# Performance work log

Hardware: AMD Instinct MI355X
Metric: run time of the kernel (lower is better)

Reference implementation:

```python
import jax, jax.numpy as jnp
import numpy as np

N, E, L, S = 20000, 100000, 128, 6   # nodes, edges, latent, message-passing steps
NF, EF, TW, OUT = 11, 5, 5, 1        # node feat, edge feat, time_window, output_size
LN_EPS = 1e-5


def _mlp_ln(x, W1, b1, W2, b2, g, beta):
    # Linear -> ReLU -> Linear -> ReLU -> LayerNorm (matches torch Sequential)
    h = jax.nn.relu(x @ W1 + b1)
    h = jax.nn.relu(h @ W2 + b2)
    mu = h.mean(-1, keepdims=True)
    var = ((h - mu) ** 2).mean(-1, keepdims=True)
    return (h - mu) * jax.lax.rsqrt(var + LN_EPS) * g + beta


def setup_inputs() -> dict:
    key = jax.random.key(0)
    ks = iter(jax.random.split(key, 64))

    def w(shape):
        fan_in = shape[-2]
        return jax.random.normal(next(ks), shape, jnp.float32) / np.float32(np.sqrt(fan_in))

    inp = {
        'node_features': jax.random.normal(next(ks), (1, N, NF), jnp.float32),
        'edge_features': jax.random.normal(next(ks), (1, E, EF), jnp.float32),
        'senders': jax.random.randint(next(ks), (E,), 0, N, jnp.int32),
        'receivers': jax.random.randint(next(ks), (E,), 0, N, jnp.int32),
        'node_mean': jax.random.normal(next(ks), (NF,), jnp.float32),
        'node_std': jnp.ones((NF,), jnp.float32),
        'edge_mean': jax.random.normal(next(ks), (EF,), jnp.float32),
        'edge_std': jnp.ones((EF,), jnp.float32),
        'enc_n_W1': w((NF, L)), 'enc_n_b1': jnp.zeros((L,), jnp.float32),
        'enc_n_W2': w((L, L)), 'enc_n_b2': jnp.zeros((L,), jnp.float32),
        'enc_n_g': jnp.ones((L,), jnp.float32), 'enc_n_beta': jnp.zeros((L,), jnp.float32),
        'enc_e_W1': w((EF, L)), 'enc_e_b1': jnp.zeros((L,), jnp.float32),
        'enc_e_W2': w((L, L)), 'enc_e_b2': jnp.zeros((L,), jnp.float32),
        'enc_e_g': jnp.ones((L,), jnp.float32), 'enc_e_beta': jnp.zeros((L,), jnp.float32),
        'blk_e_W1': w((S, 3 * L, L)), 'blk_e_b1': jnp.zeros((S, L), jnp.float32),
        'blk_e_W2': w((S, L, L)), 'blk_e_b2': jnp.zeros((S, L), jnp.float32),
        'blk_e_g': jnp.ones((S, L), jnp.float32), 'blk_e_beta': jnp.zeros((S, L), jnp.float32),
        'blk_n_W1': w((S, 2 * L, L)), 'blk_n_b1': jnp.zeros((S, L), jnp.float32),
        'blk_n_W2': w((S, L, L)), 'blk_n_b2': jnp.zeros((S, L), jnp.float32),
        'blk_n_g': jnp.ones((S, L), jnp.float32), 'blk_n_beta': jnp.zeros((S, L), jnp.float32),
        'dec_W1': w((L, 8)), 'dec_b1': jnp.zeros((8,), jnp.float32),
        'dec_W2': w((8, TW)), 'dec_b2': jnp.zeros((TW,), jnp.float32),
    }
    return inp


def reference(node_features, edge_features, senders, receivers,
              node_mean, node_std, edge_mean, edge_std,
              enc_n_W1, enc_n_b1, enc_n_W2, enc_n_b2, enc_n_g, enc_n_beta,
              enc_e_W1, enc_e_b1, enc_e_W2, enc_e_b2, enc_e_g, enc_e_beta,
              blk_e_W1, blk_e_b1, blk_e_W2, blk_e_b2, blk_e_g, blk_e_beta,
              blk_n_W1, blk_n_b1, blk_n_W2, blk_n_b2, blk_n_g, blk_n_beta,
              dec_W1, dec_b1, dec_W2, dec_b2):
    # ---- encode (Normalizer in eval mode: (x - mean) / std) ----
    node_lat = _mlp_ln((node_features - node_mean) / node_std,
                       enc_n_W1, enc_n_b1, enc_n_W2, enc_n_b2, enc_n_g, enc_n_beta)  # [1,N,L]
    edge_lat = _mlp_ln((edge_features - edge_mean) / edge_std,
                       enc_e_W1, enc_e_b1, enc_e_W2, enc_e_b2, enc_e_g, enc_e_beta)  # [1,E,L]

    # ---- process: gather -> edge MLP -> scatter_add -> node MLP, residuals ----
    for i in range(S):
        e_in = jnp.concatenate([node_lat[:, senders, :], node_lat[:, receivers, :], edge_lat], axis=-1)  # [1,E,3L]
        new_e = _mlp_ln(e_in, blk_e_W1[i], blk_e_b1[i], blk_e_W2[i], blk_e_b2[i], blk_e_g[i], blk_e_beta[i])
        aggr = jax.ops.segment_sum(new_e[0], receivers, num_segments=N)[None]  # [1,N,L]
        new_n = _mlp_ln(jnp.concatenate([node_lat, aggr], axis=-1),
                        blk_n_W1[i], blk_n_b1[i], blk_n_W2[i], blk_n_b2[i], blk_n_g[i], blk_n_beta[i])
        node_lat = node_lat + new_n
        edge_lat = edge_lat + new_e

    # ---- decode: Conv1d(k=1) == per-node linear; Swish(beta=1) ----
    h = node_lat[0] @ dec_W1 + dec_b1          # [N,8]
    h = h * jax.nn.sigmoid(h)
    dec = h @ dec_W2 + dec_b2                  # [N,TW]
    dt = jnp.repeat(jnp.arange(1, TW + 1), OUT).astype(dec.dtype)  # [TW*OUT]
    delta = (dec * dt).reshape(N, TW, OUT).transpose(1, 0, 2)      # [TW,N,OUT]
    return delta
```

## Files before the change

kernel.cpp:

```cpp
#include <hip/hip_runtime.h>
#include <cstdint>
#include <cstddef>


#define N_NODES 20000
#define N_EDGES 100000
#define LDIM    128
#define NSTEPS  6

typedef float  f32x4  __attribute__((ext_vector_type(4)));
typedef __bf16 bf16x8 __attribute__((ext_vector_type(8)));
typedef __bf16 bf16x2 __attribute__((ext_vector_type(2)));

__device__ __forceinline__ bf16x8 cvt8(const float* p) {
  float4 u = *(const float4*)p;
  float4 v = *(const float4*)(p + 4);
  bf16x8 o;
  o[0] = (__bf16)u.x; o[1] = (__bf16)u.y; o[2] = (__bf16)u.z; o[3] = (__bf16)u.w;
  o[4] = (__bf16)v.x; o[5] = (__bf16)v.y; o[6] = (__bf16)v.z; o[7] = (__bf16)v.w;
  return o;
}

struct PrepArgs {
  const float *s_enW1, *s_enW2, *s_eeW1, *s_eeW2;
  const float *s_beW1, *s_beW2, *s_bnW1, *s_bnW2;
  __bf16 *d_enW1, *d_enW2, *d_eeW1, *d_eeW2;
  __bf16 *d_beW1, *d_beW2, *d_bnW1, *d_bnW2;
  int* counts;
};

__device__ __forceinline__ void swz_src(int idx, int& k, int& col) {
  int j    = idx & 7;
  int lane = (idx >> 3) & 63;
  int ct   = (idx >> 9) & 7;
  int kc   = idx >> 12;
  col = ct * 16 + (lane & 15);
  k   = kc * 32 + (lane >> 4) * 8 + j;
}

__global__ __launch_bounds__(256) void prep_kernel(PrepArgs p) {
  int idx = blockIdx.x * 256 + threadIdx.x;
  int k, col;

  if (idx < 4096) {
    swz_src(idx, k, col);
    p.d_enW1[idx] = (__bf16)((k < 11) ? p.s_enW1[k * 128 + col] : 0.f);
    return;
  }
  idx -= 4096;
  if (idx < 16384) {
    swz_src(idx, k, col);
    p.d_enW2[idx] = (__bf16)p.s_enW2[k * 128 + col];
    return;
  }
  idx -= 16384;
  if (idx < 4096) {
    swz_src(idx, k, col);
    p.d_eeW1[idx] = (__bf16)((k < 5) ? p.s_eeW1[k * 128 + col] : 0.f);
    return;
  }
  idx -= 4096;
  if (idx < 16384) {
    swz_src(idx, k, col);
    p.d_eeW2[idx] = (__bf16)p.s_eeW2[k * 128 + col];
    return;
  }
  idx -= 16384;
  if (idx < 294912) {
    int s = idx / 49152, rem = idx % 49152;
    swz_src(rem, k, col);
    p.d_beW1[idx] = (__bf16)p.s_beW1[(size_t)s * 49152 + k * 128 + col];
    return;
  }
  idx -= 294912;
  if (idx < 98304) {
    int s = idx >> 14, rem = idx & 16383;
    swz_src(rem, k, col);
    p.d_beW2[idx] = (__bf16)p.s_beW2[s * 16384 + k * 128 + col];
    return;
  }
  idx -= 98304;
  if (idx < 196608) {
    int s = idx >> 15, rem = idx & 32767;
    swz_src(rem, k, col);
    p.d_bnW1[idx] = (__bf16)p.s_bnW1[s * 32768 + k * 128 + col];
    return;
  }
  idx -= 196608;
  if (idx < 98304) {
    int s = idx >> 14, rem = idx & 16383;
    swz_src(rem, k, col);
    p.d_bnW2[idx] = (__bf16)p.s_bnW2[s * 16384 + k * 128 + col];
    return;
  }
  idx -= 98304;
  if (idx < N_NODES) p.counts[idx] = 0;
}

__global__ __launch_bounds__(256) void hist_kernel(const int* __restrict__ recv,
                                                   int* __restrict__ counts) {
  int e = blockIdx.x * 256 + threadIdx.x;
  if (e < N_EDGES) atomicAdd(&counts[recv[e]], 1);
}

__global__ __launch_bounds__(1024) void scan_kernel(const int* __restrict__ counts,
                                                    int* __restrict__ row_ptr,
                                                    int* __restrict__ cursor) {
  __shared__ int part[1024];
  const int t = threadIdx.x;
  const int base = t * 20;
  int local[20];
  int s = 0;
#pragma unroll
  for (int i = 0; i < 20; ++i) {
    int idx = base + i;
    int v = (idx < N_NODES) ? counts[idx] : 0;
    local[i] = s;
    s += v;
  }
  part[t] = s;
  __syncthreads();
  for (int off = 1; off < 1024; off <<= 1) {
    int add = (t >= off) ? part[t - off] : 0;
    __syncthreads();
    part[t] += add;
    __syncthreads();
  }
  const int excl = part[t] - s;
#pragma unroll
  for (int i = 0; i < 20; ++i) {
    int idx = base + i;
    if (idx < N_NODES) {
      int v = excl + local[i];
      row_ptr[idx] = v;
      cursor[idx]  = v;
    }
  }
  if (t == 1023) row_ptr[N_NODES] = part[1023];
}

__global__ __launch_bounds__(256) void fill_kernel(const int* __restrict__ recv,
                                                   int* __restrict__ cursor,
                                                   int* __restrict__ edge_list) {
  int e = blockIdx.x * 256 + threadIdx.x;
  if (e < N_EDGES) {
    int r = recv[e];
    int pos = atomicAdd(&cursor[r], 1);
    edge_list[pos] = e;
  }
}

__global__ __launch_bounds__(256) void agg_kernel(
    const int* __restrict__ row_ptr, const int* __restrict__ edge_list,
    const __bf16* __restrict__ new_e, __bf16* __restrict__ aggr_bf) {
  const int wv   = threadIdx.x >> 6;
  const int lane = threadIdx.x & 63;
  const int n    = blockIdx.x * 4 + wv;
  if (n >= N_NODES) return;
  int p = row_ptr[n];
  const int pe = row_ptr[n + 1];
  float s0 = 0.f, s1 = 0.f;
  while (p < pe) {
    const int cnt = min(pe - p, 64);
    int eid = (lane < cnt) ? edge_list[p + lane] : 0;
    for (int j = 0; j < cnt; ++j) {
      const int e = __shfl(eid, j);
      bf16x2 v = *(const bf16x2*)(new_e + (size_t)e * LDIM + lane * 2);
      s0 += (float)v[0];
      s1 += (float)v[1];
    }
    p += cnt;
  }
  bf16x2 o;
  o[0] = (__bf16)s0; o[1] = (__bf16)s1;
  *(bf16x2*)(aggr_bf + (size_t)n * LDIM + lane * 2) = o;
}

struct MlpArgs {
  const float* x; const float* mean; const float* stdv;
  float* node_lat; float* edge_lat;
  __bf16* new_e;
  const __bf16* aggr_bf;
  const int* senders; const int* receivers;
  const __bf16* W1t; const __bf16* W2t;
  const float* b1; const float* b2; const float* g; const float* beta;
  int M;
};

template <int K1, int MODE>
__global__ __launch_bounds__(256, 3) void mlp2_kernel(MlpArgs a) {
  constexpr int NKC = K1 / 32;
  constexpr int RT  = 2;
  constexpr int HS  = 136;

  __shared__ __align__(16) __bf16 H1[4 * 32 * HS];

  const int tid   = threadIdx.x;
  const int lane  = tid & 63;
  const int wv    = tid >> 6;
  const int l15   = lane & 15;
  const int quad  = lane >> 4;
  const int M     = a.M;
  const int rbase = blockIdx.x * 128 + wv * 32;

  __bf16* h1w = H1 + wv * 32 * HS;

  int rowA[RT];
#pragma unroll
  for (int rt = 0; rt < RT; ++rt) {
    int r = rbase + rt * 16 + l15;
    rowA[rt] = (r < M) ? r : (M - 1);
  }

  int sA[RT], rA[RT];
  if constexpr (MODE == 2) {
#pragma unroll
    for (int rt = 0; rt < RT; ++rt) {
      sA[rt] = a.senders[rowA[rt]];
      rA[rt] = a.receivers[rowA[rt]];
    }
  }

  f32x4 acc[RT][8];
#pragma unroll
  for (int rt = 0; rt < RT; ++rt)
#pragma unroll
    for (int i = 0; i < 8; ++i) acc[rt][i] = (f32x4)(0.f);

#pragma unroll
  for (int kc = 0; kc < NKC; ++kc) {
    bf16x8 af[RT];
    if constexpr (MODE == 0 || MODE == 1) {
      constexpr int KIN = (MODE == 0) ? 11 : 5;
#pragma unroll
      for (int rt = 0; rt < RT; ++rt) {
        const float* xr = a.x + (size_t)rowA[rt] * KIN;
#pragma unroll
        for (int j = 0; j < 8; ++j) {
          int c = quad * 8 + j;
          float v = (c < KIN) ? (xr[c] - a.mean[c]) / a.stdv[c] : 0.f;
          af[rt][j] = (__bf16)v;
        }
      }
    } else if constexpr (MODE == 2) {
      if (kc < 4) {
#pragma unroll
        for (int rt = 0; rt < RT; ++rt)
          af[rt] = cvt8(a.node_lat + (size_t)sA[rt] * LDIM + kc * 32 + quad * 8);
      } else if (kc < 8) {
#pragma unroll
        for (int rt = 0; rt < RT; ++rt)
          af[rt] = cvt8(a.node_lat + (size_t)rA[rt] * LDIM + (kc - 4) * 32 + quad * 8);
      } else {
#pragma unroll
        for (int rt = 0; rt < RT; ++rt)
          af[rt] = cvt8(a.edge_lat + (size_t)rowA[rt] * LDIM + (kc - 8) * 32 + quad * 8);
      }
    } else {
      if (kc < 4) {
#pragma unroll
        for (int rt = 0; rt < RT; ++rt)
          af[rt] = cvt8(a.node_lat + (size_t)rowA[rt] * LDIM + kc * 32 + quad * 8);
      } else {
#pragma unroll
        for (int rt = 0; rt < RT; ++rt)
          af[rt] = *(const bf16x8*)(a.aggr_bf + (size_t)rowA[rt] * LDIM + (kc - 4) * 32 + quad * 8);
      }
    }

    bf16x8 bf[8];
#pragma unroll
    for (int ct = 0; ct < 8; ++ct)
      bf[ct] = *(const bf16x8*)(a.W1t + ((kc * 8 + ct) * 64 + lane) * 8);

#pragma unroll
    for (int rt = 0; rt < RT; ++rt)
#pragma unroll
      for (int ct = 0; ct < 8; ++ct)
        acc[rt][ct] = __builtin_amdgcn_mfma_f32_16x16x32_bf16(af[rt], bf[ct], acc[rt][ct], 0, 0, 0);
  }

#pragma unroll
  for (int ct = 0; ct < 8; ++ct) {
    const float bb = a.b1[ct * 16 + l15];
#pragma unroll
    for (int rt = 0; rt < RT; ++rt)
#pragma unroll
      for (int rr = 0; rr < 4; ++rr) {
        float v = fmaxf(acc[rt][ct][rr] + bb, 0.f);
        h1w[(rt * 16 + quad * 4 + rr) * HS + ct * 16 + l15] = (__bf16)v;
      }
  }

#pragma unroll
  for (int rt = 0; rt < RT; ++rt)
#pragma unroll
    for (int i = 0; i < 8; ++i) acc[rt][i] = (f32x4)(0.f);

#pragma unroll
  for (int kc = 0; kc < 4; ++kc) {
    bf16x8 af[RT];
#pragma unroll
    for (int rt = 0; rt < RT; ++rt)
      af[rt] = *(const bf16x8*)(h1w + (rt * 16 + l15) * HS + kc * 32 + quad * 8);
    bf16x8 bf[8];
#pragma unroll
    for (int ct = 0; ct < 8; ++ct)
      bf[ct] = *(const bf16x8*)(a.W2t + ((kc * 8 + ct) * 64 + lane) * 8);
#pragma unroll
    for (int rt = 0; rt < RT; ++rt)
#pragma unroll
      for (int ct = 0; ct < 8; ++ct)
        acc[rt][ct] = __builtin_amdgcn_mfma_f32_16x16x32_bf16(af[rt], bf[ct], acc[rt][ct], 0, 0, 0);
  }

#pragma unroll
  for (int ct = 0; ct < 8; ++ct) {
    const float bb = a.b2[ct * 16 + l15];
#pragma unroll
    for (int rt = 0; rt < RT; ++rt)
#pragma unroll
      for (int rr = 0; rr < 4; ++rr)
        acc[rt][ct][rr] = fmaxf(acc[rt][ct][rr] + bb, 0.f);
  }

  float mu[RT][4], rs[RT][4];
#pragma unroll
  for (int rt = 0; rt < RT; ++rt)
#pragma unroll
    for (int rr = 0; rr < 4; ++rr) {
      float s = 0.f, s2 = 0.f;
#pragma unroll
      for (int ct = 0; ct < 8; ++ct) { float v = acc[rt][ct][rr]; s += v; s2 += v * v; }
      s  += __shfl_xor(s, 1);  s2 += __shfl_xor(s2, 1);
      s  += __shfl_xor(s, 2);  s2 += __shfl_xor(s2, 2);
      s  += __shfl_xor(s, 4);  s2 += __shfl_xor(s2, 4);
      s  += __shfl_xor(s, 8);  s2 += __shfl_xor(s2, 8);
      float m = s * (1.f / 128.f);
      float var = fmaxf(s2 * (1.f / 128.f) - m * m, 0.f);
      mu[rt][rr] = m; rs[rt][rr] = rsqrtf(var + 1e-5f);
    }

  float gv[8], bev[8];
#pragma unroll
  for (int ct = 0; ct < 8; ++ct) {
    gv[ct]  = a.g[ct * 16 + l15];
    bev[ct] = a.beta[ct * 16 + l15];
  }

#pragma unroll
  for (int rt = 0; rt < RT; ++rt)
#pragma unroll
    for (int rr = 0; rr < 4; ++rr) {
      const int row = rbase + rt * 16 + quad * 4 + rr;
      if (row >= M) continue;
      if constexpr (MODE == 2) {
#pragma unroll
        for (int ct = 0; ct < 8; ++ct) {
          const int col = ct * 16 + l15;
          float y = (acc[rt][ct][rr] - mu[rt][rr]) * rs[rt][rr] * gv[ct] + bev[ct];
          a.edge_lat[(size_t)row * LDIM + col] += y;
          a.new_e[(size_t)row * LDIM + col] = (__bf16)y;
        }
      } else {
#pragma unroll
        for (int ct = 0; ct < 8; ++ct) {
          const int col = ct * 16 + l15;
          float y = (acc[rt][ct][rr] - mu[rt][rr]) * rs[rt][rr] * gv[ct] + bev[ct];
          if constexpr (MODE == 0)      a.node_lat[(size_t)row * LDIM + col] = y;
          else if constexpr (MODE == 1) a.edge_lat[(size_t)row * LDIM + col] = y;
          else                          a.node_lat[(size_t)row * LDIM + col] += y;
        }
      }
    }
}

__global__ __launch_bounds__(256) void decode_kernel(
    const float* __restrict__ node_lat,
    const float* __restrict__ W1, const float* __restrict__ b1,
    const float* __restrict__ W2, const float* __restrict__ b2,
    float* __restrict__ out) {
  __shared__ float X[64][129];
  const int n0 = blockIdx.x * 64;
  for (int idx = threadIdx.x; idx < 64 * 32; idx += 256) {
    int r = idx >> 5, c4 = idx & 31;
    int n = n0 + r; if (n >= N_NODES) n = N_NODES - 1;
    float4 v = *((const float4*)(node_lat + (size_t)n * 128) + c4);
    X[r][c4 * 4 + 0] = v.x; X[r][c4 * 4 + 1] = v.y;
    X[r][c4 * 4 + 2] = v.z; X[r][c4 * 4 + 3] = v.w;
  }
  __syncthreads();
  const int r = threadIdx.x;
  if (r < 64) {
    const int n = n0 + r;
    if (n < N_NODES) {
      float h[8];
#pragma unroll
      for (int j = 0; j < 8; ++j) h[j] = b1[j];
      for (int k = 0; k < 128; ++k) {
        float xv = X[r][k];
#pragma unroll
        for (int j = 0; j < 8; ++j) h[j] = fmaf(xv, W1[k * 8 + j], h[j]);
      }
#pragma unroll
      for (int j = 0; j < 8; ++j) h[j] = h[j] / (1.f + expf(-h[j]));
#pragma unroll
      for (int t = 0; t < 5; ++t) {
        float d = b2[t];
#pragma unroll
        for (int j = 0; j < 8; ++j) d = fmaf(h[j], W2[j * 5 + t], d);
        out[t * N_NODES + n] = d * (float)(t + 1);
      }
    }
  }
}

extern "C" void kernel_launch(void* const* d_in, const int* in_sizes, int n_in,
                              void* d_out, int out_size, void* d_ws, size_t ws_size,
                              hipStream_t stream) {
  (void)in_sizes; (void)n_in; (void)out_size; (void)ws_size;

  const float* node_features = (const float*)d_in[0];
  const float* edge_features = (const float*)d_in[1];
  const int*   senders       = (const int*)d_in[2];
  const int*   receivers     = (const int*)d_in[3];
  const float* node_mean = (const float*)d_in[4];
  const float* node_std  = (const float*)d_in[5];
  const float* edge_mean = (const float*)d_in[6];
  const float* edge_std  = (const float*)d_in[7];
  const float* enc_n_W1 = (const float*)d_in[8];
  const float* enc_n_b1 = (const float*)d_in[9];
  const float* enc_n_W2 = (const float*)d_in[10];
  const float* enc_n_b2 = (const float*)d_in[11];
  const float* enc_n_g    = (const float*)d_in[12];
  const float* enc_n_beta = (const float*)d_in[13];
  const float* enc_e_W1 = (const float*)d_in[14];
  const float* enc_e_b1 = (const float*)d_in[15];
  const float* enc_e_W2 = (const float*)d_in[16];
  const float* enc_e_b2 = (const float*)d_in[17];
  const float* enc_e_g    = (const float*)d_in[18];
  const float* enc_e_beta = (const float*)d_in[19];
  const float* blk_e_W1 = (const float*)d_in[20];
  const float* blk_e_b1 = (const float*)d_in[21];
  const float* blk_e_W2 = (const float*)d_in[22];
  const float* blk_e_b2 = (const float*)d_in[23];
  const float* blk_e_g    = (const float*)d_in[24];
  const float* blk_e_beta = (const float*)d_in[25];
  const float* blk_n_W1 = (const float*)d_in[26];
  const float* blk_n_b1 = (const float*)d_in[27];
  const float* blk_n_W2 = (const float*)d_in[28];
  const float* blk_n_b2 = (const float*)d_in[29];
  const float* blk_n_g    = (const float*)d_in[30];
  const float* blk_n_beta = (const float*)d_in[31];
  const float* dec_W1 = (const float*)d_in[32];
  const float* dec_b1 = (const float*)d_in[33];
  const float* dec_W2 = (const float*)d_in[34];
  const float* dec_b2 = (const float*)d_in[35];

  char* ws = (char*)d_ws;
  float*  node_lat = (float*)(ws);
  float*  edge_lat = (float*)(ws + 10240000);
  __bf16* new_e    = (__bf16*)(ws + 61440000);
  __bf16* wb       = (__bf16*)(ws + 87040000);
  int* counts    = (int*)(ws + 88498176);
  int* row_ptr   = (int*)(ws + 88578176);
  int* cursor    = (int*)(ws + 88658192);
  int* edge_list = (int*)(ws + 88738192);
  __bf16* aggr_bf = (__bf16*)(ws + 89138192);

  __bf16* enW1s = wb;
  __bf16* enW2s = enW1s + 4096;
  __bf16* eeW1s = enW2s + 16384;
  __bf16* eeW2s = eeW1s + 4096;
  __bf16* beW1s = eeW2s + 16384;
  __bf16* beW2s = beW1s + 6 * 49152;
  __bf16* bnW1s = beW2s + 6 * 16384;
  __bf16* bnW2s = bnW1s + 6 * 32768;

  PrepArgs pa;
  pa.s_enW1 = enc_n_W1; pa.s_enW2 = enc_n_W2; pa.s_eeW1 = enc_e_W1; pa.s_eeW2 = enc_e_W2;
  pa.s_beW1 = blk_e_W1; pa.s_beW2 = blk_e_W2; pa.s_bnW1 = blk_n_W1; pa.s_bnW2 = blk_n_W2;
  pa.d_enW1 = enW1s; pa.d_enW2 = enW2s; pa.d_eeW1 = eeW1s; pa.d_eeW2 = eeW2s;
  pa.d_beW1 = beW1s; pa.d_beW2 = beW2s; pa.d_bnW1 = bnW1s; pa.d_bnW2 = bnW2s;
  pa.counts = counts;
  prep_kernel<<<2927, 256, 0, stream>>>(pa);

  hist_kernel<<<(N_EDGES + 255) / 256, 256, 0, stream>>>(receivers, counts);
  scan_kernel<<<1, 1024, 0, stream>>>(counts, row_ptr, cursor);
  fill_kernel<<<(N_EDGES + 255) / 256, 256, 0, stream>>>(receivers, cursor, edge_list);

  const int NODE_BLOCKS = (N_NODES + 127) / 128;
  const int EDGE_BLOCKS = (N_EDGES + 127) / 128;
  const int DEC_BLOCKS  = (N_NODES + 63) / 64;
  const int AGG_BLOCKS  = (N_NODES + 3) / 4;

  MlpArgs base;
  base.node_lat = node_lat; base.edge_lat = edge_lat; base.new_e = new_e;
  base.aggr_bf = aggr_bf;
  base.senders = senders; base.receivers = receivers;
  base.x = nullptr; base.mean = nullptr; base.stdv = nullptr;

  {
    MlpArgs a = base;
    a.x = node_features; a.mean = node_mean; a.stdv = node_std;
    a.W1t = enW1s; a.W2t = enW2s;
    a.b1 = enc_n_b1; a.b2 = enc_n_b2; a.g = enc_n_g; a.beta = enc_n_beta;
    a.M = N_NODES;
    mlp2_kernel<32, 0><<<NODE_BLOCKS, 256, 0, stream>>>(a);
  }
  {
    MlpArgs a = base;
    a.x = edge_features; a.mean = edge_mean; a.stdv = edge_std;
    a.W1t = eeW1s; a.W2t = eeW2s;
    a.b1 = enc_e_b1; a.b2 = enc_e_b2; a.g = enc_e_g; a.beta = enc_e_beta;
    a.M = N_EDGES;
    mlp2_kernel<32, 1><<<EDGE_BLOCKS, 256, 0, stream>>>(a);
  }

  for (int i = 0; i < NSTEPS; ++i) {
    {
      MlpArgs a = base;
      a.W1t = beW1s + (size_t)i * 49152; a.W2t = beW2s + (size_t)i * 16384;
      a.b1 = blk_e_b1 + i * 128; a.b2 = blk_e_b2 + i * 128;
      a.g = blk_e_g + i * 128; a.beta = blk_e_beta + i * 128;
      a.M = N_EDGES;
      mlp2_kernel<384, 2><<<EDGE_BLOCKS, 256, 0, stream>>>(a);
    }
    agg_kernel<<<AGG_BLOCKS, 256, 0, stream>>>(row_ptr, edge_list, new_e, aggr_bf);
    {
      MlpArgs a = base;
      a.W1t = bnW1s + (size_t)i * 32768; a.W2t = bnW2s + (size_t)i * 16384;
      a.b1 = blk_n_b1 + i * 128; a.b2 = blk_n_b2 + i * 128;
      a.g = blk_n_g + i * 128; a.beta = blk_n_beta + i * 128;
      a.M = N_NODES;
      mlp2_kernel<256, 3><<<NODE_BLOCKS, 256, 0, stream>>>(a);
    }
  }

  decode_kernel<<<DEC_BLOCKS, 256, 0, stream>>>(
      node_lat, dec_W1, dec_b1, dec_W2, dec_b2, (float*)d_out);
}
```

Baseline: 782.2 us.

## Use single-wave MLP blocks and batch activation gathers per 128-wide phase

Each MLP block now holds a single 64-thread wavefront handling 32 rows instead of four waves handling 128, and the grid grows to match. The first GEMM's activation loads are regrouped so that all four k-chunks of a 128-wide segment (sender, receiver, edge, or aggr) are issued before the MFMAs run. This exposes more memory-level parallelism per wave for the gather loads. In exchange, register pressure rises because more fragments are live at once, and with launch_bounds(64,3) occupancy now depends on per-block LDS and the VGPR count.

```diff
diff --git a/kernel.cpp b/kernel.cpp
--- a/kernel.cpp
+++ b/kernel.cpp
@@ -188,22 +188,20 @@
 };
 
 template <int K1, int MODE>
-__global__ __launch_bounds__(256, 3) void mlp2_kernel(MlpArgs a) {
+__global__ __launch_bounds__(64, 3) void mlp2_kernel(MlpArgs a) {
   constexpr int NKC = K1 / 32;
   constexpr int RT  = 2;
   constexpr int HS  = 136;
 
-  __shared__ __align__(16) __bf16 H1[4 * 32 * HS];
-
-  const int tid   = threadIdx.x;
-  const int lane  = tid & 63;
-  const int wv    = tid >> 6;
+  __shared__ __align__(16) __bf16 H1[32 * HS];
+
+  const int lane  = threadIdx.x & 63;
   const int l15   = lane & 15;
   const int quad  = lane >> 4;
   const int M     = a.M;
-  const int rbase = blockIdx.x * 128 + wv * 32;
-
-  __bf16* h1w = H1 + wv * 32 * HS;
+  const int rbase = blockIdx.x * 32;
+
+  __bf16* h1w = H1;
 
   int rowA[RT];
 #pragma unroll
@@ -227,57 +225,64 @@
 #pragma unroll
     for (int i = 0; i < 8; ++i) acc[rt][i] = (f32x4)(0.f);
 
-#pragma unroll
-  for (int kc = 0; kc < NKC; ++kc) {
+  if constexpr (MODE == 0 || MODE == 1) {
+    constexpr int KIN = (MODE == 0) ? 11 : 5;
     bf16x8 af[RT];
-    if constexpr (MODE == 0 || MODE == 1) {
-      constexpr int KIN = (MODE == 0) ? 11 : 5;
-#pragma unroll
-      for (int rt = 0; rt < RT; ++rt) {
-        const float* xr = a.x + (size_t)rowA[rt] * KIN;
-#pragma unroll
-        for (int j = 0; j < 8; ++j) {
-          int c = quad * 8 + j;
-          float v = (c < KIN) ? (xr[c] - a.mean[c]) / a.stdv[c] : 0.f;
-          af[rt][j] = (__bf16)v;
+#pragma unroll
+    for (int rt = 0; rt < RT; ++rt) {
+      const float* xr = a.x + (size_t)rowA[rt] * KIN;
+#pragma unroll
+      for (int j = 0; j < 8; ++j) {
+        int c = quad * 8 + j;
+        float v = (c < KIN) ? (xr[c] - a.mean[c]) / a.stdv[c] : 0.f;
+        af[rt][j] = (__bf16)v;
+      }
+    }
+    bf16x8 bfv[8];
+#pragma unroll
+    for (int ct = 0; ct < 8; ++ct)
+      bfv[ct] = *(const bf16x8*)(a.W1t + (ct * 64 + lane) * 8);
+#pragma unroll
+    for (int rt = 0; rt < RT; ++rt)
+#pragma unroll
+      for (int ct = 0; ct < 8; ++ct)
+        acc[rt][ct] = __builtin_amdgcn_mfma_f32_16x16x32_bf16(af[rt], bfv[ct], acc[rt][ct], 0, 0, 0);
+  } else {
+    constexpr int NPH = NKC / 4;
+#pragma unroll
+    for (int ph = 0; ph < NPH; ++ph) {
+      bf16x8 afr[RT][4];
+#pragma unroll
+      for (int kk = 0; kk < 4; ++kk) {
+#pragma unroll
+        for (int rt = 0; rt < RT; ++rt) {
+          if constexpr (MODE == 2) {
+            const float* src = (ph == 0) ? (a.node_lat + (size_t)sA[rt] * LDIM)
+                             : (ph == 1) ? (a.node_lat + (size_t)rA[rt] * LDIM)
+                                         : (a.edge_lat + (size_t)rowA[rt] * LDIM);
+            afr[rt][kk] = cvt8(src + kk * 32 + quad * 8);
+          } else {
+            if (ph == 0)
+              afr[rt][kk] = cvt8(a.node_lat + (size_t)rowA[rt] * LDIM + kk * 32 + quad * 8);
+            else
+              afr[rt][kk] = *(const bf16x8*)(a.aggr_bf + (size_t)rowA[rt] * LDIM + kk * 32 + quad * 8);
+          }
         }
       }
-    } else if constexpr (MODE == 2) {
-      if (kc < 4) {
+#pragma unroll
+      for (int kk = 0; kk < 4; ++kk) {
+        const int kc = ph * 4 + kk;
+        bf16x8 bfv[8];
+#pragma unroll
+        for (int ct = 0; ct < 8; ++ct)
+          bfv[ct] = *(const bf16x8*)(a.W1t + ((kc * 8 + ct) * 64 + lane) * 8);
 #pragma unroll
         for (int rt = 0; rt < RT; ++rt)
-          af[rt] = cvt8(a.node_lat + (size_t)sA[rt] * LDIM + kc * 32 + quad * 8);
-      } else if (kc < 8) {
-#pragma unroll
-        for (int rt = 0; rt < RT; ++rt)
-          af[rt] = cvt8(a.node_lat + (size_t)rA[rt] * LDIM + (kc - 4) * 32 + quad * 8);
-      } else {
-#pragma unroll
-        for (int rt = 0; rt < RT; ++rt)
-          af[rt] = cvt8(a.edge_lat + (size_t)rowA[rt] * LDIM + (kc - 8) * 32 + quad * 8);
-      }
-    } else {
-      if (kc < 4) {
-#pragma unroll
-        for (int rt = 0; rt < RT; ++rt)
-          af[rt] = cvt8(a.node_lat + (size_t)rowA[rt] * LDIM + kc * 32 + quad * 8);
-      } else {
-#pragma unroll
-        for (int rt = 0; rt < RT; ++rt)
-          af[rt] = *(const bf16x8*)(a.aggr_bf + (size_t)rowA[rt] * LDIM + (kc - 4) * 32 + quad * 8);
-      }
-    }
-
-    bf16x8 bf[8];
-#pragma unroll
-    for (int ct = 0; ct < 8; ++ct)
-      bf[ct] = *(const bf16x8*)(a.W1t + ((kc * 8 + ct) * 64 + lane) * 8);
-
-#pragma unroll
-    for (int rt = 0; rt < RT; ++rt)
-#pragma unroll
-      for (int ct = 0; ct < 8; ++ct)
-        acc[rt][ct] = __builtin_amdgcn_mfma_f32_16x16x32_bf16(af[rt], bf[ct], acc[rt][ct], 0, 0, 0);
+#pragma unroll
+          for (int ct = 0; ct < 8; ++ct)
+            acc[rt][ct] = __builtin_amdgcn_mfma_f32_16x16x32_bf16(afr[rt][kk], bfv[ct], acc[rt][ct], 0, 0, 0);
+      }
+    }
   }
 
 #pragma unroll
@@ -303,15 +308,15 @@
 #pragma unroll
     for (int rt = 0; rt < RT; ++rt)
       af[rt] = *(const bf16x8*)(h1w + (rt * 16 + l15) * HS + kc * 32 + quad * 8);
-    bf16x8 bf[8];
+    bf16x8 bfv[8];
 #pragma unroll
     for (int ct = 0; ct < 8; ++ct)
-      bf[ct] = *(const bf16x8*)(a.W2t + ((kc * 8 + ct) * 64 + lane) * 8);
+      bfv[ct] = *(const bf16x8*)(a.W2t + ((kc * 8 + ct) * 64 + lane) * 8);
 #pragma unroll
     for (int rt = 0; rt < RT; ++rt)
 #pragma unroll
       for (int ct = 0; ct < 8; ++ct)
-        acc[rt][ct] = __builtin_amdgcn_mfma_f32_16x16x32_bf16(af[rt], bf[ct], acc[rt][ct], 0, 0, 0);
+        acc[rt][ct] = __builtin_amdgcn_mfma_f32_16x16x32_bf16(af[rt], bfv[ct], acc[rt][ct], 0, 0, 0);
   }
 
 #pragma unroll
@@ -489,8 +494,8 @@
   scan_kernel<<<1, 1024, 0, stream>>>(counts, row_ptr, cursor);
   fill_kernel<<<(N_EDGES + 255) / 256, 256, 0, stream>>>(receivers, cursor, edge_list);
 
-  const int NODE_BLOCKS = (N_NODES + 127) / 128;
-  const int EDGE_BLOCKS = (N_EDGES + 127) / 128;
+  const int NODE_BLOCKS = (N_NODES + 31) / 32;
+  const int EDGE_BLOCKS = (N_EDGES + 31) / 32;
   const int DEC_BLOCKS  = (N_NODES + 63) / 64;
   const int AGG_BLOCKS  = (N_NODES + 3) / 4;
 
@@ -506,7 +511,7 @@
     a.W1t = enW1s; a.W2t = enW2s;
     a.b1 = enc_n_b1; a.b2 = enc_n_b2; a.g = enc_n_g; a.beta = enc_n_beta;
     a.M = N_NODES;
-    mlp2_kernel<32, 0><<<NODE_BLOCKS, 256, 0, stream>>>(a);
+    mlp2_kernel<32, 0><<<NODE_BLOCKS, 64, 0, stream>>>(a);
   }
   {
     MlpArgs a = base;
@@ -514,7 +519,7 @@
     a.W1t = eeW1s; a.W2t = eeW2s;
     a.b1 = enc_e_b1; a.b2 = enc_e_b2; a.g = enc_e_g; a.beta = enc_e_beta;
     a.M = N_EDGES;
-    mlp2_kernel<32, 1><<<EDGE_BLOCKS, 256, 0, stream>>>(a);
+    mlp2_kernel<32, 1><<<EDGE_BLOCKS, 64, 0, stream>>>(a);
   }
 
   for (int i = 0; i < NSTEPS; ++i) {
@@ -524,7 +529,7 @@
       a.b1 = blk_e_b1 + i * 128; a.b2 = blk_e_b2 + i * 128;
       a.g = blk_e_g + i * 128; a.beta = blk_e_beta + i * 128;
       a.M = N_EDGES;
-      mlp2_kernel<384, 2><<<EDGE_BLOCKS, 256, 0, stream>>>(a);
+      mlp2_kernel<384, 2><<<EDGE_BLOCKS, 64, 0, stream>>>(a);
     }
     agg_kernel<<<AGG_BLOCKS, 256, 0, stream>>>(row_ptr, edge_list, new_e, aggr_bf);
     {
@@ -533,7 +538,7 @@
       a.b1 = blk_n_b1 + i * 128; a.b2 = blk_n_b2 + i * 128;
       a.g = blk_n_g + i * 128; a.beta = blk_n_beta + i * 128;
       a.M = N_NODES;
-      mlp2_kernel<256, 3><<<NODE_BLOCKS, 256, 0, stream>>>(a);
+      mlp2_kernel<256, 3><<<NODE_BLOCKS, 64, 0, stream>>>(a);
     }
   }
 
```

Result: faster. 706.9 us (-9.6%).
